# Kernel tuning notes

Measured on AMD Instinct MI355X. Metric: run time of the kernel, lower is better.

## Reference

```python
import jax, jax.numpy as jnp
import numpy as np
from jax import lax

# --- config (matches init_kwargs) ---
H = 1024          # hidden_size
I = 704           # moe_intermediate_size (per expert)
E = 32            # n_routed_experts
G = 8             # n_group
TOPK_GROUP = 3    # topk_group
K = 6             # num_experts_per_tok
N_SHARED = 2      # n_shared_experts -> shared intermediate = N_SHARED * I
SCALE = 1.0       # routed_scaling_factor
T = 2048          # number of tokens
CAP = 2 * (T * K) // E


def setup_inputs() -> dict:
    key = jax.random.key(0)
    ks = jax.random.split(key, 8)
    s = 0.02  # initializer_range
    Is = N_SHARED * I
    return {
        "x": jax.random.normal(ks[0], (T, H), jnp.float32),
        "gate_w": s * jax.random.normal(ks[1], (E, H), jnp.float32),   # router
        "w_gate": s * jax.random.normal(ks[2], (E, H, I), jnp.float32),
        "w_up":   s * jax.random.normal(ks[3], (E, H, I), jnp.float32),
        "w_down": s * jax.random.normal(ks[4], (E, I, H), jnp.float32),
        "sw_gate": s * jax.random.normal(ks[5], (H, Is), jnp.float32),
        "sw_up":   s * jax.random.normal(ks[6], (H, Is), jnp.float32),
        "sw_down": s * jax.random.normal(ks[7], (Is, H), jnp.float32),
    }


def _moe_forward(x, gate_w, w_gate, w_up, w_down, sw_gate, sw_up, sw_down):
    # ---- router: softmax scores + group-limited top-k (topk_method='gready') ----
    logits = x @ gate_w.T                                  # [T, E]
    scores = jax.nn.softmax(logits, axis=-1)               # [T, E]
    group_scores = scores.reshape(T, G, E // G).max(-1)    # [T, G]
    _, gidx = lax.top_k(group_scores, TOPK_GROUP)          # [T, topk_group]
    gmask = jnp.zeros((T, G), scores.dtype).at[jnp.arange(T)[:, None], gidx].set(1.0)
    emask = jnp.repeat(gmask, E // G, axis=1)              # [T, E]
    masked_scores = jnp.where(emask > 0, scores, 0.0)
    topk_w, topk_idx = lax.top_k(masked_scores, K)         # [T, K]
    # norm_topk_prob=False -> weights are raw softmax scores * routed_scaling_factor
    topk_w = topk_w * SCALE

    # ---- dispatch: sort assignments by expert, scatter into [E, CAP, H] buffers ----
    flat_e = topk_idx.reshape(-1)                          # [T*K]
    order = jnp.argsort(flat_e)
    se = flat_e[order]                                     # sorted expert ids
    tok = order // K                                       # source token of each slot
    counts = jax.ops.segment_sum(jnp.ones_like(flat_e), flat_e, num_segments=E)
    starts = jnp.cumsum(counts) - counts
    pos = jnp.arange(T * K) - starts[se]                   # position within expert
    valid = pos < CAP
    pos_w = jnp.where(valid, pos, CAP)                     # overflow slot CAP (sliced off)
    xbuf = jnp.zeros((E, CAP + 1, H), x.dtype).at[se, pos_w].set(x[tok])
    xb = xbuf[:, :CAP]                                     # [E, CAP, H]

    # ---- grouped expert MLPs: silu(x Wg) * (x Wu) @ Wd ----
    g = jnp.einsum("ech,ehi->eci", xb, w_gate)
    u = jnp.einsum("ech,ehi->eci", xb, w_up)
    yb = jnp.einsum("eci,eih->ech", jax.nn.silu(g) * u, w_down)  # [E, CAP, H]

    # ---- combine: gather back and weighted-scatter to tokens ----
    y_flat = yb[se, jnp.minimum(pos, CAP - 1)] * valid[:, None].astype(x.dtype)
    wts = topk_w.reshape(-1)[order]                        # [T*K]
    routed = jnp.zeros((T, H), x.dtype).at[tok].add(y_flat * wts[:, None])

    # ---- shared experts MLP (intermediate = n_shared * moe_inter) ----
    sg = jax.nn.silu(x @ sw_gate) * (x @ sw_up)
    shared = sg @ sw_down

    return routed + shared                                 # [T, H]


def reference(x, gate_w, w_gate, w_up, w_down, sw_gate, sw_up, sw_down):
    return _moe_forward(x, gate_w, w_gate, w_up, w_down, sw_gate, sw_up, sw_down)
```

## Files before the change

### kernel.cpp

```cpp
#include <hip/hip_runtime.h>
#include <hip/hip_bf16.h>

#define H 1024
#define I_DIM 704
#define E 32
#define TOPK_GROUP 3
#define K_TOP 6
#define T_TOK 2048
#define CAP 768
#define IS_DIM 1408
#define NCHUNK 192

typedef __attribute__((ext_vector_type(8))) short short8v;
typedef __attribute__((ext_vector_type(4))) float f32x4;

__device__ __forceinline__ unsigned short f2bfbits(float f) {
  unsigned u = __float_as_uint(f);
  unsigned r = (u + 0x7fffu + ((u >> 16) & 1u)) >> 16;
  return (unsigned short)r;
}
__device__ __forceinline__ unsigned packbf2(float lo, float hi) {
  __hip_bfloat162 h = __float22bfloat162_rn(make_float2(lo, hi));
  unsigned u; __builtin_memcpy(&u, &h, 4); return u;
}
__device__ __forceinline__ float bf2f(unsigned short b) {
  return __uint_as_float(((unsigned)b) << 16);
}
__device__ __forceinline__ void gload_lds16(const short* g, short* l) {
  __builtin_amdgcn_global_load_lds(
      (const __attribute__((address_space(1))) unsigned int*)g,
      (__attribute__((address_space(3))) unsigned int*)l, 16, 0, 0);
}

__global__ void cast_x_kernel(const float* __restrict__ x, short* __restrict__ xb) {
  size_t i = ((size_t)blockIdx.x * 256 + threadIdx.x) * 4;
  float4 v = *(const float4*)(x + i);
  short4 s;
  s.x = (short)f2bfbits(v.x); s.y = (short)f2bfbits(v.y);
  s.z = (short)f2bfbits(v.z); s.w = (short)f2bfbits(v.w);
  *(short4*)(xb + i) = s;
}

__global__ __launch_bounds__(64) void gating_kernel(const float* __restrict__ x,
                                                    const float* __restrict__ gw,
                                                    int* __restrict__ tidx,
                                                    float* __restrict__ tw) {
  int t = blockIdx.x;
  int lane = threadIdx.x;
  int e = lane & 31, half = lane >> 5;
  const float4* xr4 = (const float4*)(x + (size_t)t * H + half * 512);
  const float4* wr4 = (const float4*)(gw + (size_t)e * H + half * 512);
  double acc = 0.0;
  #pragma unroll 4
  for (int j = 0; j < 128; ++j) {
    float4 a = xr4[j], b = wr4[j];
    acc += (double)a.x * b.x + (double)a.y * b.y + (double)a.z * b.z + (double)a.w * b.w;
  }
  acc += __shfl_down(acc, 32);
  double lg = acc;
  double m = lg;
  #pragma unroll
  for (int off = 16; off >= 1; off >>= 1) {
    double o = __shfl_xor(m, off);
    if (o > m) m = o;
  }
  double p = exp(lg - m);
  double sum = p;
  #pragma unroll
  for (int off = 16; off >= 1; off >>= 1) sum += __shfl_xor(sum, off);
  p /= sum;
  double gmax = p;
  { double o = __shfl_xor(gmax, 1); if (o > gmax) gmax = o;
    o = __shfl_xor(gmax, 2); if (o > gmax) gmax = o; }
  bool gsel = false;
  double gv = gmax;
  #pragma unroll
  for (int it = 0; it < TOPK_GROUP; ++it) {
    double v = gv; int gi = e >> 2;
    #pragma unroll
    for (int off = 16; off >= 1; off >>= 1) {
      double ov = __shfl_xor(v, off);
      int oi = __shfl_xor(gi, off);
      if (ov > v || (ov == v && oi < gi)) { v = ov; gi = oi; }
    }
    if ((e >> 2) == gi) { gsel = true; gv = -1e300; }
  }
  double mp = gsel ? p : 0.0;
  #pragma unroll
  for (int it = 0; it < K_TOP; ++it) {
    double v = mp; int ei = e;
    #pragma unroll
    for (int off = 16; off >= 1; off >>= 1) {
      double ov = __shfl_xor(v, off);
      int oi = __shfl_xor(ei, off);
      if (ov > v || (ov == v && oi < ei)) { v = ov; ei = oi; }
    }
    if (lane == 0) { tidx[t * K_TOP + it] = ei; tw[t * K_TOP + it] = (float)v; }
    if (e == ei) mp = -2.0;
  }
}

__global__ __launch_bounds__(64) void hist_kernel(const int* __restrict__ tidx,
                                                  int* __restrict__ chunk_hist) {
  __shared__ int h[E];
  int c = blockIdx.x, lane = threadIdx.x;
  if (lane < E) h[lane] = 0;
  __syncthreads();
  int te = tidx[c * 64 + lane];
  atomicAdd(&h[te], 1);
  __syncthreads();
  if (lane < E) chunk_hist[c * E + lane] = h[lane];
}

__global__ __launch_bounds__(1024) void scan_kernel(const int* __restrict__ chunk_hist,
                                                    int* __restrict__ chunk_base,
                                                    int* __restrict__ cnt) {
  __shared__ int h[NCHUNK * E];
  int t = threadIdx.x;
  for (int i = t; i < NCHUNK * E; i += 1024) h[i] = chunk_hist[i];
  __syncthreads();
  if (t < E) {
    int run = 0;
    for (int c = 0; c < NCHUNK; ++c) {
      int v = h[c * E + t];
      h[c * E + t] = run;
      run += v;
    }
    cnt[t] = run < CAP ? run : CAP;
  }
  __syncthreads();
  for (int i = t; i < NCHUNK * E; i += 1024) chunk_base[i] = h[i];
}

__global__ __launch_bounds__(64) void place_kernel(const int* __restrict__ tidx,
                                                   const int* __restrict__ chunk_base,
                                                   int* __restrict__ token_list,
                                                   int* __restrict__ sid) {
  int c = blockIdx.x, lane = threadIdx.x;
  int idx = c * 64 + lane;
  int te = tidx[idx];
  unsigned long long mymask = 0;
  #pragma unroll
  for (int e = 0; e < E; ++e) {
    unsigned long long bal = __ballot(te == e);
    if (te == e) mymask = bal;
  }
  int rank = __popcll(mymask & ((1ull << lane) - 1ull));
  int pos = chunk_base[c * E + te] + rank;
  int s = -1;
  if (pos < CAP) {
    token_list[te * CAP + pos] = idx / K_TOP;
    s = te * CAP + pos;
  }
  sid[idx] = s;
}

__global__ __launch_bounds__(256) void gateup_kernel(
    const short* __restrict__ Xb, const float* __restrict__ Wg, const float* __restrict__ Wu,
    short* __restrict__ Sout, const int* __restrict__ tlist, const int* __restrict__ cnt_dev,
    int Nld, long long wstride, long long sstride) {
  int e = blockIdx.z;
  int cnt = cnt_dev ? cnt_dev[e] : T_TOK;
  int row0 = blockIdx.y * 128;
  if (row0 >= cnt) return;
  int col0 = blockIdx.x * 64;
  const float* wg = Wg + (long long)e * wstride;
  const float* wu = Wu + (long long)e * wstride;
  short* sbase = Sout + (long long)e * sstride;

  __shared__ __align__(16) short As[2][128 * 32];
  __shared__ __align__(16) short Bgs[64 * 32];
  __shared__ __align__(16) short Bus[64 * 32];

  int tid = threadIdx.x;
  int lane = tid & 63, wave = tid >> 6;

  int rr = tid >> 2, ch = tid & 3;
  int che = ch ^ ((rr >> 1) & 3);
  int ra0 = row0 + rr, ra1 = ra0 + 64;
  if (tlist) {
    const int* tl = tlist + e * CAP;
    ra0 = tl[min(ra0, cnt - 1)];
    ra1 = tl[min(ra1, cnt - 1)];
  }
  const short* pa0 = Xb + (size_t)ra0 * H + che * 8;
  const short* pa1 = Xb + (size_t)ra1 * H + che * 8;
  short* ldsA00 = &As[0][(wave * 16) * 32];
  short* ldsA10 = &As[0][(64 + wave * 16) * 32];
  short* ldsA01 = &As[1][(wave * 16) * 32];
  short* ldsA11 = &As[1][(64 + wave * 16) * 32];

  int bn = lane;
  const float* pg = wg + (size_t)(wave * 8) * Nld + col0 + bn;
  const float* pu = wu + (size_t)(wave * 8) * Nld + col0 + bn;
  int kswz = (wave ^ ((bn >> 1) & 3)) * 8;
  short* ldsBg = &Bgs[bn * 32 + kswz];
  short* ldsBu = &Bus[bn * 32 + kswz];

  int wm = wave & 1, wn = wave >> 1;
  int c = lane & 15, q = lane >> 4;
  int qa = q ^ ((c >> 1) & 3);
  const short* fA0 = &As[0][(wm * 64 + c) * 32 + qa * 8];
  const short* fA1 = &As[1][(wm * 64 + c) * 32 + qa * 8];
  const short* fBg = &Bgs[(wn * 32 + c) * 32 + qa * 8];
  const short* fBu = &Bus[(wn * 32 + c) * 32 + qa * 8];

  f32x4 accg[4][2], accu[4][2];
  #pragma unroll
  for (int i = 0; i < 4; ++i)
    #pragma unroll
    for (int j = 0; j < 2; ++j) {
      accg[i][j] = (f32x4){0.f, 0.f, 0.f, 0.f};
      accu[i][j] = (f32x4){0.f, 0.f, 0.f, 0.f};
    }

  float gvA[8], uvA[8], gvB[8], uvB[8];
  gload_lds16(pa0, ldsA00);
  gload_lds16(pa1, ldsA10);
  #pragma unroll
  for (int j = 0; j < 8; ++j) {
    gvA[j] = pg[(size_t)j * Nld];
    uvA[j] = pu[(size_t)j * Nld];
  }

#define GU_PHASE(KC, FAC, LA0, LA1, GC, UC, GN, UN, PREF)                           \
  {                                                                                 \
    __builtin_amdgcn_s_barrier();                                                   \
    asm volatile("" ::: "memory");                                                  \
    if (PREF) {                                                                     \
      gload_lds16(pa0 + (KC) + 32, LA0);                                            \
      gload_lds16(pa1 + (KC) + 32, LA1);                                            \
      const float* pgk = pg + (size_t)((KC) + 32) * Nld;                            \
      const float* puk = pu + (size_t)((KC) + 32) * Nld;                            \
      _Pragma("unroll")                                                             \
      for (int j = 0; j < 8; ++j) {                                                 \
        GN[j] = pgk[(size_t)j * Nld];                                               \
        UN[j] = puk[(size_t)j * Nld];                                               \
      }                                                                             \
    }                                                                               \
    uint4 wvg, wvu;                                                                 \
    wvg.x = packbf2(GC[0], GC[1]); wvg.y = packbf2(GC[2], GC[3]);                   \
    wvg.z = packbf2(GC[4], GC[5]); wvg.w = packbf2(GC[6], GC[7]);                   \
    wvu.x = packbf2(UC[0], UC[1]); wvu.y = packbf2(UC[2], UC[3]);                   \
    wvu.z = packbf2(UC[4], UC[5]); wvu.w = packbf2(UC[6], UC[7]);                   \
    *(uint4*)ldsBg = wvg;                                                           \
    *(uint4*)ldsBu = wvu;                                                           \
    asm volatile("s_waitcnt lgkmcnt(0)" ::: "memory");                              \
    asm volatile("s_waitcnt vmcnt(18)" ::: "memory");                               \
    __builtin_amdgcn_s_barrier();                                                   \
    __builtin_amdgcn_sched_barrier(0);                                              \
    short8v a[4], bg[2], bu[2];                                                     \
    _Pragma("unroll")                                                               \
    for (int mi = 0; mi < 4; ++mi) a[mi] = *(const short8v*)((FAC) + mi * 16 * 32); \
    _Pragma("unroll")                                                               \
    for (int ni = 0; ni < 2; ++ni) {                                                \
      bg[ni] = *(const short8v*)(fBg + ni * 16 * 32);                               \
      bu[ni] = *(const short8v*)(fBu + ni * 16 * 32);                               \
    }                                                                               \
    _Pragma("unroll")                                                               \
    for (int mi = 0; mi < 4; ++mi)                                                  \
      _Pragma("unroll")                                                             \
      for (int ni = 0; ni < 2; ++ni) {                                              \
        accg[mi][ni] = __builtin_amdgcn_mfma_f32_16x16x32_bf16(a[mi], bg[ni], accg[mi][ni], 0, 0, 0); \
        accu[mi][ni] = __builtin_amdgcn_mfma_f32_16x16x32_bf16(a[mi], bu[ni], accu[mi][ni], 0, 0, 0); \
      }                                                                             \
  }

  for (int k0 = 0; k0 < H; k0 += 64) {
    GU_PHASE(k0,      fA0, ldsA01, ldsA11, gvA, uvA, gvB, uvB, true);
    GU_PHASE(k0 + 32, fA1, ldsA00, ldsA10, gvB, uvB, gvA, uvA, (k0 + 64 < H));
  }
#undef GU_PHASE

  #pragma unroll
  for (int mi = 0; mi < 4; ++mi) {
    int rbase = row0 + wm * 64 + mi * 16 + q * 4;
    #pragma unroll
    for (int ni = 0; ni < 2; ++ni) {
      int col = col0 + wn * 32 + ni * 16 + c;
      #pragma unroll
      for (int r = 0; r < 4; ++r) {
        float g = accg[mi][ni][r], u = accu[mi][ni][r];
        float s = (g / (1.f + __expf(-g))) * u;
        sbase[(size_t)(rbase + r) * Nld + col] = (short)f2bfbits(s);
      }
    }
  }
}

__global__ __launch_bounds__(256) void down_kernel(
    const short* __restrict__ Sin, const float* __restrict__ Wd,
    float* __restrict__ outF, short* __restrict__ outY,
    const int* __restrict__ cnt_dev, int Kdim, long long wstride, long long sstride) {
  int e = blockIdx.z;
  int cnt = cnt_dev ? cnt_dev[e] : T_TOK;
  int row0 = blockIdx.y * 128;
  if (row0 >= cnt) return;
  int col0 = blockIdx.x * 128;
  const short* sb = Sin + (long long)e * sstride;
  const float* wd = Wd + (long long)e * wstride;

  __shared__ __align__(16) short As[2][128 * 32];
  __shared__ __align__(16) short Bs[128 * 32];

  int tid = threadIdx.x;
  int lane = tid & 63, wave = tid >> 6;
  int rr = tid >> 2, ch = tid & 3;
  int che = ch ^ ((rr >> 1) & 3);

  const short* pa0 = sb + (size_t)(row0 + rr) * Kdim + che * 8;
  const short* pa1 = pa0 + (size_t)64 * Kdim;
  short* ldsA00 = &As[0][(wave * 16) * 32];
  short* ldsA10 = &As[0][(64 + wave * 16) * 32];
  short* ldsA01 = &As[1][(wave * 16) * 32];
  short* ldsA11 = &As[1][(64 + wave * 16) * 32];

  int bn = tid & 127, w2 = tid >> 7;
  const float* pb = wd + (size_t)(w2 * 16) * H + col0 + bn;
  int bs = (bn >> 1) & 3;
  short* ldsB0 = &Bs[bn * 32 + ((w2 * 2) ^ bs) * 8];
  short* ldsB1 = &Bs[bn * 32 + ((w2 * 2 + 1) ^ bs) * 8];

  int wm = wave & 1, wn = wave >> 1;
  int c = lane & 15, q = lane >> 4;
  int qa = q ^ ((c >> 1) & 3);
  const short* fA0 = &As[0][(wm * 64 + c) * 32 + qa * 8];
  const short* fA1 = &As[1][(wm * 64 + c) * 32 + qa * 8];
  const short* fB  = &Bs[(wn * 64 + c) * 32 + qa * 8];

  f32x4 acc[4][4];
  #pragma unroll
  for (int i = 0; i < 4; ++i)
    #pragma unroll
    for (int j = 0; j < 4; ++j) acc[i][j] = (f32x4){0.f, 0.f, 0.f, 0.f};

  float bvA[16], bvB[16];
  gload_lds16(pa0, ldsA00);
  gload_lds16(pa1, ldsA10);
  #pragma unroll
  for (int j = 0; j < 16; ++j) bvA[j] = pb[(size_t)j * H];

#define DN_PHASE(KC, FAC, LA0, LA1, BC, BND, PREF)                                  \
  {                                                                                 \
    __builtin_amdgcn_s_barrier();                                                   \
    asm volatile("" ::: "memory");                                                  \
    if (PREF) {                                                                     \
      gload_lds16(pa0 + (KC) + 32, LA0);                                            \
      gload_lds16(pa1 + (KC) + 32, LA1);                                            \
      const float* pbk = pb + (size_t)((KC) + 32) * H;                              \
      _Pragma("unroll")                                                             \
      for (int j = 0; j < 16; ++j) BND[j] = pbk[(size_t)j * H];                     \
    }                                                                               \
    uint4 w0, w1;                                                                   \
    w0.x = packbf2(BC[0], BC[1]);   w0.y = packbf2(BC[2], BC[3]);                   \
    w0.z = packbf2(BC[4], BC[5]);   w0.w = packbf2(BC[6], BC[7]);                   \
    w1.x = packbf2(BC[8], BC[9]);   w1.y = packbf2(BC[10], BC[11]);                 \
    w1.z = packbf2(BC[12], BC[13]); w1.w = packbf2(BC[14], BC[15]);                 \
    *(uint4*)ldsB0 = w0;                                                            \
    *(uint4*)ldsB1 = w1;                                                            \
    asm volatile("s_waitcnt lgkmcnt(0)" ::: "memory");                              \
    asm volatile("s_waitcnt vmcnt(18)" ::: "memory");                               \
    __builtin_amdgcn_s_barrier();                                                   \
    __builtin_amdgcn_sched_barrier(0);                                              \
    short8v a[4], b[4];                                                             \
    _Pragma("unroll")                                                               \
    for (int mi = 0; mi < 4; ++mi) a[mi] = *(const short8v*)((FAC) + mi * 16 * 32); \
    _Pragma("unroll")                                                               \
    for (int ni = 0; ni < 4; ++ni) b[ni] = *(const short8v*)(fB + ni * 16 * 32);    \
    _Pragma("unroll")                                                               \
    for (int mi = 0; mi < 4; ++mi)                                                  \
      _Pragma("unroll")                                                             \
      for (int ni = 0; ni < 4; ++ni)                                                \
        acc[mi][ni] = __builtin_amdgcn_mfma_f32_16x16x32_bf16(a[mi], b[ni], acc[mi][ni], 0, 0, 0); \
  }

  for (int k0 = 0; k0 < Kdim; k0 += 64) {
    DN_PHASE(k0,      fA0, ldsA01, ldsA11, bvA, bvB, true);
    DN_PHASE(k0 + 32, fA1, ldsA00, ldsA10, bvB, bvA, (k0 + 64 < Kdim));
  }
#undef DN_PHASE

  if (outY) {
    #pragma unroll
    for (int mi = 0; mi < 4; ++mi) {
      int rb = row0 + wm * 64 + mi * 16 + q * 4;
      #pragma unroll
      for (int r = 0; r < 4; ++r) {
        short* yrow = outY + (size_t)(e * CAP + rb + r) * H;
        #pragma unroll
        for (int ni = 0; ni < 4; ++ni) {
          int col = col0 + wn * 64 + ni * 16 + c;
          yrow[col] = (short)f2bfbits(acc[mi][ni][r]);
        }
      }
    }
  } else {
    #pragma unroll
    for (int mi = 0; mi < 4; ++mi) {
      int rb = row0 + wm * 64 + mi * 16 + q * 4;
      #pragma unroll
      for (int ni = 0; ni < 4; ++ni) {
        int col = col0 + wn * 64 + ni * 16 + c;
        #pragma unroll
        for (int r = 0; r < 4; ++r)
          outF[(size_t)(rb + r) * H + col] = acc[mi][ni][r];
      }
    }
  }
}

__global__ __launch_bounds__(256) void combine_kernel(
    const short* __restrict__ Yr, const int* __restrict__ sid,
    const float* __restrict__ twt, float* __restrict__ out) {
  int t = blockIdx.x;
  int col = threadIdx.x * 4;
  float* op = out + (size_t)t * H + col;
  float4 o = *(float4*)op;
  #pragma unroll
  for (int k = 0; k < K_TOP; ++k) {
    int s = sid[t * K_TOP + k];
    if (s >= 0) {
      float w = twt[t * K_TOP + k];
      ushort4 y = *(const ushort4*)(Yr + (size_t)s * H + col);
      o.x += w * bf2f(y.x);
      o.y += w * bf2f(y.y);
      o.z += w * bf2f(y.z);
      o.w += w * bf2f(y.w);
    }
  }
  *(float4*)op = o;
}

extern "C" void kernel_launch(void* const* d_in, const int* in_sizes, int n_in,
                              void* d_out, int out_size, void* d_ws, size_t ws_size,
                              hipStream_t stream) {
  const float* x       = (const float*)d_in[0];
  const float* gate_w  = (const float*)d_in[1];
  const float* w_gate  = (const float*)d_in[2];
  const float* w_up    = (const float*)d_in[3];
  const float* w_down  = (const float*)d_in[4];
  const float* sw_gate = (const float*)d_in[5];
  const float* sw_up   = (const float*)d_in[6];
  const float* sw_down = (const float*)d_in[7];
  float* out = (float*)d_out;
  char* ws = (char*)d_ws;

  size_t o = 0;
  short* xb   = (short*)(ws + o); o += (size_t)T_TOK * H * 2;
  short* Sr   = (short*)(ws + o); o += (size_t)E * CAP * I_DIM * 2;
  short* Ss   = (short*)(ws + o); o += (size_t)T_TOK * IS_DIM * 2;
  short* Yr   = (short*)(ws + o); o += (size_t)E * CAP * H * 2;
  int*   tidx = (int*)(ws + o);   o += (size_t)T_TOK * K_TOP * 4;
  float* twt  = (float*)(ws + o); o += (size_t)T_TOK * K_TOP * 4;
  int*   sid  = (int*)(ws + o);   o += (size_t)T_TOK * K_TOP * 4;
  int*   tl   = (int*)(ws + o);   o += (size_t)E * CAP * 4;
  int*   cnt  = (int*)(ws + o);   o += 256;
  int*   chist = (int*)(ws + o);  o += (size_t)NCHUNK * E * 4;
  int*   cbase = (int*)(ws + o);  o += (size_t)NCHUNK * E * 4;

  cast_x_kernel<<<(T_TOK * H) / 1024, 256, 0, stream>>>(x, xb);
  gating_kernel<<<T_TOK, 64, 0, stream>>>(x, gate_w, tidx, twt);
  hist_kernel<<<NCHUNK, 64, 0, stream>>>(tidx, chist);
  scan_kernel<<<1, 1024, 0, stream>>>(chist, cbase, cnt);
  place_kernel<<<NCHUNK, 64, 0, stream>>>(tidx, cbase, tl, sid);

  gateup_kernel<<<dim3(I_DIM / 64, CAP / 128, E), 256, 0, stream>>>(
      xb, w_gate, w_up, Sr, tl, cnt, I_DIM, (long long)H * I_DIM, (long long)CAP * I_DIM);
  gateup_kernel<<<dim3(IS_DIM / 64, T_TOK / 128, 1), 256, 0, stream>>>(
      xb, sw_gate, sw_up, Ss, nullptr, nullptr, IS_DIM, 0, 0);
  down_kernel<<<dim3(H / 128, T_TOK / 128, 1), 256, 0, stream>>>(
      Ss, sw_down, out, nullptr, nullptr, IS_DIM, 0, 0);
  down_kernel<<<dim3(H / 128, CAP / 128, E), 256, 0, stream>>>(
      Sr, w_down, nullptr, Yr, cnt, I_DIM, (long long)I_DIM * H, (long long)CAP * I_DIM);
  combine_kernel<<<T_TOK, 256, 0, stream>>>(Yr, sid, twt, out);
}
```

Measured before the change: 548.0 us.

## Pre-transpose weights to bf16 and stream B tiles via direct-to-LDS loads

Adds a tiled transpose-and-cast kernel that converts every expert and shared weight matrix from fp32 [K,N] to bf16 [N,K] on each call. The gate/up and down GEMMs then load B tiles with the same global_load_lds path as A, double-buffered in LDS. This removes the per-thread strided fp32 loads, register staging and bf16 packing from the GEMM inner loop. The cost is an extra full pass over all weights every call, plus more workspace, with the transposed gate weights aliased onto the Yr buffer.

```diff
diff --git a/kernel.cpp b/kernel.cpp
--- a/kernel.cpp
+++ b/kernel.cpp
@@ -19,10 +19,6 @@
   unsigned r = (u + 0x7fffu + ((u >> 16) & 1u)) >> 16;
   return (unsigned short)r;
 }
-__device__ __forceinline__ unsigned packbf2(float lo, float hi) {
-  __hip_bfloat162 h = __float22bfloat162_rn(make_float2(lo, hi));
-  unsigned u; __builtin_memcpy(&u, &h, 4); return u;
-}
 __device__ __forceinline__ float bf2f(unsigned short b) {
   return __uint_as_float(((unsigned)b) << 16);
 }
@@ -39,6 +35,38 @@
   s.x = (short)f2bfbits(v.x); s.y = (short)f2bfbits(v.y);
   s.z = (short)f2bfbits(v.z); s.w = (short)f2bfbits(v.w);
   *(short4*)(xb + i) = s;
+}
+
+__global__ __launch_bounds__(256) void tw_kernel(const float* __restrict__ in,
+                                                 short* __restrict__ out,
+                                                 int K, int N) {
+  __shared__ float tile[64][65];
+  long long eoff = (long long)blockIdx.z * (long long)K * N;
+  const float* ip = in + eoff;
+  short* op = out + eoff;
+  int n0 = blockIdx.x * 64, k0 = blockIdx.y * 64;
+  int t = threadIdx.x;
+  int tr = t >> 4;
+  int tc = (t & 15) * 4;
+  #pragma unroll
+  for (int i = 0; i < 4; ++i) {
+    float4 v = *(const float4*)(ip + (size_t)(k0 + tr + i * 16) * N + n0 + tc);
+    tile[tr + i * 16][tc + 0] = v.x;
+    tile[tr + i * 16][tc + 1] = v.y;
+    tile[tr + i * 16][tc + 2] = v.z;
+    tile[tr + i * 16][tc + 3] = v.w;
+  }
+  __syncthreads();
+  #pragma unroll
+  for (int i = 0; i < 4; ++i) {
+    int n = tr + i * 16;
+    short4 s;
+    s.x = (short)f2bfbits(tile[tc + 0][n]);
+    s.y = (short)f2bfbits(tile[tc + 1][n]);
+    s.z = (short)f2bfbits(tile[tc + 2][n]);
+    s.w = (short)f2bfbits(tile[tc + 3][n]);
+    *(short4*)(op + (size_t)(n0 + n) * K + k0 + tc) = s;
+  }
 }
 
 __global__ __launch_bounds__(64) void gating_kernel(const float* __restrict__ x,
@@ -156,7 +184,7 @@
 }
 
 __global__ __launch_bounds__(256) void gateup_kernel(
-    const short* __restrict__ Xb, const float* __restrict__ Wg, const float* __restrict__ Wu,
+    const short* __restrict__ Xb, const short* __restrict__ Wg, const short* __restrict__ Wu,
     short* __restrict__ Sout, const int* __restrict__ tlist, const int* __restrict__ cnt_dev,
     int Nld, long long wstride, long long sstride) {
   int e = blockIdx.z;
@@ -164,13 +192,13 @@
   int row0 = blockIdx.y * 128;
   if (row0 >= cnt) return;
   int col0 = blockIdx.x * 64;
-  const float* wg = Wg + (long long)e * wstride;
-  const float* wu = Wu + (long long)e * wstride;
+  const short* wg = Wg + (long long)e * wstride;
+  const short* wu = Wu + (long long)e * wstride;
   short* sbase = Sout + (long long)e * sstride;
 
   __shared__ __align__(16) short As[2][128 * 32];
-  __shared__ __align__(16) short Bgs[64 * 32];
-  __shared__ __align__(16) short Bus[64 * 32];
+  __shared__ __align__(16) short Bgs[2][64 * 32];
+  __shared__ __align__(16) short Bus[2][64 * 32];
 
   int tid = threadIdx.x;
   int lane = tid & 63, wave = tid >> 6;
@@ -185,25 +213,27 @@
   }
   const short* pa0 = Xb + (size_t)ra0 * H + che * 8;
   const short* pa1 = Xb + (size_t)ra1 * H + che * 8;
+  const short* pbg = wg + (size_t)(col0 + rr) * H + che * 8;
+  const short* pbu = wu + (size_t)(col0 + rr) * H + che * 8;
+
   short* ldsA00 = &As[0][(wave * 16) * 32];
   short* ldsA10 = &As[0][(64 + wave * 16) * 32];
   short* ldsA01 = &As[1][(wave * 16) * 32];
   short* ldsA11 = &As[1][(64 + wave * 16) * 32];
-
-  int bn = lane;
-  const float* pg = wg + (size_t)(wave * 8) * Nld + col0 + bn;
-  const float* pu = wu + (size_t)(wave * 8) * Nld + col0 + bn;
-  int kswz = (wave ^ ((bn >> 1) & 3)) * 8;
-  short* ldsBg = &Bgs[bn * 32 + kswz];
-  short* ldsBu = &Bus[bn * 32 + kswz];
+  short* ldsBg0 = &Bgs[0][(wave * 16) * 32];
+  short* ldsBg1 = &Bgs[1][(wave * 16) * 32];
+  short* ldsBu0 = &Bus[0][(wave * 16) * 32];
+  short* ldsBu1 = &Bus[1][(wave * 16) * 32];
 
   int wm = wave & 1, wn = wave >> 1;
   int c = lane & 15, q = lane >> 4;
   int qa = q ^ ((c >> 1) & 3);
-  const short* fA0 = &As[0][(wm * 64 + c) * 32 + qa * 8];
-  const short* fA1 = &As[1][(wm * 64 + c) * 32 + qa * 8];
-  const short* fBg = &Bgs[(wn * 32 + c) * 32 + qa * 8];
-  const short* fBu = &Bus[(wn * 32 + c) * 32 + qa * 8];
+  const short* fA0  = &As[0][(wm * 64 + c) * 32 + qa * 8];
+  const short* fA1  = &As[1][(wm * 64 + c) * 32 + qa * 8];
+  const short* fBg0 = &Bgs[0][(wn * 32 + c) * 32 + qa * 8];
+  const short* fBg1 = &Bgs[1][(wn * 32 + c) * 32 + qa * 8];
+  const short* fBu0 = &Bus[0][(wn * 32 + c) * 32 + qa * 8];
+  const short* fBu1 = &Bus[1][(wn * 32 + c) * 32 + qa * 8];
 
   f32x4 accg[4][2], accu[4][2];
   #pragma unroll
@@ -214,48 +244,33 @@
       accu[i][j] = (f32x4){0.f, 0.f, 0.f, 0.f};
     }
 
-  float gvA[8], uvA[8], gvB[8], uvB[8];
   gload_lds16(pa0, ldsA00);
   gload_lds16(pa1, ldsA10);
-  #pragma unroll
-  for (int j = 0; j < 8; ++j) {
-    gvA[j] = pg[(size_t)j * Nld];
-    uvA[j] = pu[(size_t)j * Nld];
-  }
-
-#define GU_PHASE(KC, FAC, LA0, LA1, GC, UC, GN, UN, PREF)                           \
+  gload_lds16(pbg, ldsBg0);
+  gload_lds16(pbu, ldsBu0);
+
+#define GU_PHASE(KC, FAc, FBGc, FBUc, A0d, A1d, BGd, BUd, PREF)                     \
   {                                                                                 \
     __builtin_amdgcn_s_barrier();                                                   \
     asm volatile("" ::: "memory");                                                  \
     if (PREF) {                                                                     \
-      gload_lds16(pa0 + (KC) + 32, LA0);                                            \
-      gload_lds16(pa1 + (KC) + 32, LA1);                                            \
-      const float* pgk = pg + (size_t)((KC) + 32) * Nld;                            \
-      const float* puk = pu + (size_t)((KC) + 32) * Nld;                            \
-      _Pragma("unroll")                                                             \
-      for (int j = 0; j < 8; ++j) {                                                 \
-        GN[j] = pgk[(size_t)j * Nld];                                               \
-        UN[j] = puk[(size_t)j * Nld];                                               \
-      }                                                                             \
+      gload_lds16(pa0 + (KC) + 32, A0d);                                            \
+      gload_lds16(pa1 + (KC) + 32, A1d);                                            \
+      gload_lds16(pbg + (KC) + 32, BGd);                                            \
+      gload_lds16(pbu + (KC) + 32, BUd);                                            \
+      asm volatile("s_waitcnt vmcnt(4)" ::: "memory");                              \
+    } else {                                                                        \
+      asm volatile("s_waitcnt vmcnt(0)" ::: "memory");                              \
     }                                                                               \
-    uint4 wvg, wvu;                                                                 \
-    wvg.x = packbf2(GC[0], GC[1]); wvg.y = packbf2(GC[2], GC[3]);                   \
-    wvg.z = packbf2(GC[4], GC[5]); wvg.w = packbf2(GC[6], GC[7]);                   \
-    wvu.x = packbf2(UC[0], UC[1]); wvu.y = packbf2(UC[2], UC[3]);                   \
-    wvu.z = packbf2(UC[4], UC[5]); wvu.w = packbf2(UC[6], UC[7]);                   \
-    *(uint4*)ldsBg = wvg;                                                           \
-    *(uint4*)ldsBu = wvu;                                                           \
-    asm volatile("s_waitcnt lgkmcnt(0)" ::: "memory");                              \
-    asm volatile("s_waitcnt vmcnt(18)" ::: "memory");                               \
     __builtin_amdgcn_s_barrier();                                                   \
     __builtin_amdgcn_sched_barrier(0);                                              \
     short8v a[4], bg[2], bu[2];                                                     \
     _Pragma("unroll")                                                               \
-    for (int mi = 0; mi < 4; ++mi) a[mi] = *(const short8v*)((FAC) + mi * 16 * 32); \
+    for (int mi = 0; mi < 4; ++mi) a[mi] = *(const short8v*)((FAc) + mi * 16 * 32); \
     _Pragma("unroll")                                                               \
     for (int ni = 0; ni < 2; ++ni) {                                                \
-      bg[ni] = *(const short8v*)(fBg + ni * 16 * 32);                               \
-      bu[ni] = *(const short8v*)(fBu + ni * 16 * 32);                               \
+      bg[ni] = *(const short8v*)((FBGc) + ni * 16 * 32);                            \
+      bu[ni] = *(const short8v*)((FBUc) + ni * 16 * 32);                            \
     }                                                                               \
     _Pragma("unroll")                                                               \
     for (int mi = 0; mi < 4; ++mi)                                                  \
@@ -267,8 +282,8 @@
   }
 
   for (int k0 = 0; k0 < H; k0 += 64) {
-    GU_PHASE(k0,      fA0, ldsA01, ldsA11, gvA, uvA, gvB, uvB, true);
-    GU_PHASE(k0 + 32, fA1, ldsA00, ldsA10, gvB, uvB, gvA, uvA, (k0 + 64 < H));
+    GU_PHASE(k0,      fA0, fBg0, fBu0, ldsA01, ldsA11, ldsBg1, ldsBu1, true);
+    GU_PHASE(k0 + 32, fA1, fBg1, fBu1, ldsA00, ldsA10, ldsBg0, ldsBu0, (k0 + 64 < H));
   }
 #undef GU_PHASE
 
@@ -289,7 +304,7 @@
 }
 
 __global__ __launch_bounds__(256) void down_kernel(
-    const short* __restrict__ Sin, const float* __restrict__ Wd,
+    const short* __restrict__ Sin, const short* __restrict__ Wd,
     float* __restrict__ outF, short* __restrict__ outY,
     const int* __restrict__ cnt_dev, int Kdim, long long wstride, long long sstride) {
   int e = blockIdx.z;
@@ -298,10 +313,10 @@
   if (row0 >= cnt) return;
   int col0 = blockIdx.x * 128;
   const short* sb = Sin + (long long)e * sstride;
-  const float* wd = Wd + (long long)e * wstride;
+  const short* wd = Wd + (long long)e * wstride;
 
   __shared__ __align__(16) short As[2][128 * 32];
-  __shared__ __align__(16) short Bs[128 * 32];
+  __shared__ __align__(16) short Bs[2][128 * 32];
 
   int tid = threadIdx.x;
   int lane = tid & 63, wave = tid >> 6;
@@ -310,23 +325,25 @@
 
   const short* pa0 = sb + (size_t)(row0 + rr) * Kdim + che * 8;
   const short* pa1 = pa0 + (size_t)64 * Kdim;
+  const short* pb0 = wd + (size_t)(col0 + rr) * Kdim + che * 8;
+  const short* pb1 = pb0 + (size_t)64 * Kdim;
+
   short* ldsA00 = &As[0][(wave * 16) * 32];
   short* ldsA10 = &As[0][(64 + wave * 16) * 32];
   short* ldsA01 = &As[1][(wave * 16) * 32];
   short* ldsA11 = &As[1][(64 + wave * 16) * 32];
-
-  int bn = tid & 127, w2 = tid >> 7;
-  const float* pb = wd + (size_t)(w2 * 16) * H + col0 + bn;
-  int bs = (bn >> 1) & 3;
-  short* ldsB0 = &Bs[bn * 32 + ((w2 * 2) ^ bs) * 8];
-  short* ldsB1 = &Bs[bn * 32 + ((w2 * 2 + 1) ^ bs) * 8];
+  short* ldsB00 = &Bs[0][(wave * 16) * 32];
+  short* ldsB10 = &Bs[0][(64 + wave * 16) * 32];
+  short* ldsB01 = &Bs[1][(wave * 16) * 32];
+  short* ldsB11 = &Bs[1][(64 + wave * 16) * 32];
 
   int wm = wave & 1, wn = wave >> 1;
   int c = lane & 15, q = lane >> 4;
   int qa = q ^ ((c >> 1) & 3);
   const short* fA0 = &As[0][(wm * 64 + c) * 32 + qa * 8];
   const short* fA1 = &As[1][(wm * 64 + c) * 32 + qa * 8];
-  const short* fB  = &Bs[(wn * 64 + c) * 32 + qa * 8];
+  const short* fB0 = &Bs[0][(wn * 64 + c) * 32 + qa * 8];
+  const short* fB1 = &Bs[1][(wn * 64 + c) * 32 + qa * 8];
 
   f32x4 acc[4][4];
   #pragma unroll
@@ -334,39 +351,31 @@
     #pragma unroll
     for (int j = 0; j < 4; ++j) acc[i][j] = (f32x4){0.f, 0.f, 0.f, 0.f};
 
-  float bvA[16], bvB[16];
   gload_lds16(pa0, ldsA00);
   gload_lds16(pa1, ldsA10);
-  #pragma unroll
-  for (int j = 0; j < 16; ++j) bvA[j] = pb[(size_t)j * H];
-
-#define DN_PHASE(KC, FAC, LA0, LA1, BC, BND, PREF)                                  \
+  gload_lds16(pb0, ldsB00);
+  gload_lds16(pb1, ldsB10);
+
+#define DN_PHASE(KC, FAc, FBc, A0d, A1d, B0d, B1d, PREF)                            \
   {                                                                                 \
     __builtin_amdgcn_s_barrier();                                                   \
     asm volatile("" ::: "memory");                                                  \
     if (PREF) {                                                                     \
-      gload_lds16(pa0 + (KC) + 32, LA0);                                            \
-      gload_lds16(pa1 + (KC) + 32, LA1);                                            \
-      const float* pbk = pb + (size_t)((KC) + 32) * H;                              \
-      _Pragma("unroll")                                                             \
-      for (int j = 0; j < 16; ++j) BND[j] = pbk[(size_t)j * H];                     \
+      gload_lds16(pa0 + (KC) + 32, A0d);                                            \
+      gload_lds16(pa1 + (KC) + 32, A1d);                                            \
+      gload_lds16(pb0 + (KC) + 32, B0d);                                            \
+      gload_lds16(pb1 + (KC) + 32, B1d);                                            \
+      asm volatile("s_waitcnt vmcnt(4)" ::: "memory");                              \
+    } else {                                                                        \
+      asm volatile("s_waitcnt vmcnt(0)" ::: "memory");                              \
     }                                                                               \
-    uint4 w0, w1;                                                                   \
-    w0.x = packbf2(BC[0], BC[1]);   w0.y = packbf2(BC[2], BC[3]);                   \
-    w0.z = packbf2(BC[4], BC[5]);   w0.w = packbf2(BC[6], BC[7]);                   \
-    w1.x = packbf2(BC[8], BC[9]);   w1.y = packbf2(BC[10], BC[11]);                 \
-    w1.z = packbf2(BC[12], BC[13]); w1.w = packbf2(BC[14], BC[15]);                 \
-    *(uint4*)ldsB0 = w0;                                                            \
-    *(uint4*)ldsB1 = w1;                                                            \
-    asm volatile("s_waitcnt lgkmcnt(0)" ::: "memory");                              \
-    asm volatile("s_waitcnt vmcnt(18)" ::: "memory");                               \
     __builtin_amdgcn_s_barrier();                                                   \
     __builtin_amdgcn_sched_barrier(0);                                              \
     short8v a[4], b[4];                                                             \
     _Pragma("unroll")                                                               \
-    for (int mi = 0; mi < 4; ++mi) a[mi] = *(const short8v*)((FAC) + mi * 16 * 32); \
-    _Pragma("unroll")                                                               \
-    for (int ni = 0; ni < 4; ++ni) b[ni] = *(const short8v*)(fB + ni * 16 * 32);    \
+    for (int mi = 0; mi < 4; ++mi) a[mi] = *(const short8v*)((FAc) + mi * 16 * 32); \
+    _Pragma("unroll")                                                               \
+    for (int ni = 0; ni < 4; ++ni) b[ni] = *(const short8v*)((FBc) + ni * 16 * 32); \
     _Pragma("unroll")                                                               \
     for (int mi = 0; mi < 4; ++mi)                                                  \
       _Pragma("unroll")                                                             \
@@ -375,8 +384,8 @@
   }
 
   for (int k0 = 0; k0 < Kdim; k0 += 64) {
-    DN_PHASE(k0,      fA0, ldsA01, ldsA11, bvA, bvB, true);
-    DN_PHASE(k0 + 32, fA1, ldsA00, ldsA10, bvB, bvA, (k0 + 64 < Kdim));
+    DN_PHASE(k0,      fA0, fB0, ldsA01, ldsA11, ldsB01, ldsB11, true);
+    DN_PHASE(k0 + 32, fA1, fB1, ldsA00, ldsA10, ldsB00, ldsB10, (k0 + 64 < Kdim));
   }
 #undef DN_PHASE
 
@@ -449,7 +458,13 @@
   short* xb   = (short*)(ws + o); o += (size_t)T_TOK * H * 2;
   short* Sr   = (short*)(ws + o); o += (size_t)E * CAP * I_DIM * 2;
   short* Ss   = (short*)(ws + o); o += (size_t)T_TOK * IS_DIM * 2;
-  short* Yr   = (short*)(ws + o); o += (size_t)E * CAP * H * 2;
+  short* wg_t = (short*)(ws + o);
+  short* Yr   = (short*)(ws + o); o += (size_t)E * H * I_DIM * 2;
+  short* wu_t = (short*)(ws + o); o += (size_t)E * H * I_DIM * 2;
+  short* wd_t = (short*)(ws + o); o += (size_t)E * I_DIM * H * 2;
+  short* swg_t = (short*)(ws + o); o += (size_t)H * IS_DIM * 2;
+  short* swu_t = (short*)(ws + o); o += (size_t)H * IS_DIM * 2;
+  short* swd_t = (short*)(ws + o); o += (size_t)IS_DIM * H * 2;
   int*   tidx = (int*)(ws + o);   o += (size_t)T_TOK * K_TOP * 4;
   float* twt  = (float*)(ws + o); o += (size_t)T_TOK * K_TOP * 4;
   int*   sid  = (int*)(ws + o);   o += (size_t)T_TOK * K_TOP * 4;
@@ -464,13 +479,20 @@
   scan_kernel<<<1, 1024, 0, stream>>>(chist, cbase, cnt);
   place_kernel<<<NCHUNK, 64, 0, stream>>>(tidx, cbase, tl, sid);
 
+  tw_kernel<<<dim3(I_DIM / 64, H / 64, E), 256, 0, stream>>>(w_gate, wg_t, H, I_DIM);
+  tw_kernel<<<dim3(I_DIM / 64, H / 64, E), 256, 0, stream>>>(w_up,   wu_t, H, I_DIM);
+  tw_kernel<<<dim3(H / 64, I_DIM / 64, E), 256, 0, stream>>>(w_down, wd_t, I_DIM, H);
+  tw_kernel<<<dim3(IS_DIM / 64, H / 64, 1), 256, 0, stream>>>(sw_gate, swg_t, H, IS_DIM);
+  tw_kernel<<<dim3(IS_DIM / 64, H / 64, 1), 256, 0, stream>>>(sw_up,   swu_t, H, IS_DIM);
+  tw_kernel<<<dim3(H / 64, IS_DIM / 64, 1), 256, 0, stream>>>(sw_down, swd_t, IS_DIM, H);
+
   gateup_kernel<<<dim3(I_DIM / 64, CAP / 128, E), 256, 0, stream>>>(
-      xb, w_gate, w_up, Sr, tl, cnt, I_DIM, (long long)H * I_DIM, (long long)CAP * I_DIM);
+      xb, wg_t, wu_t, Sr, tl, cnt, I_DIM, (long long)H * I_DIM, (long long)CAP * I_DIM);
   gateup_kernel<<<dim3(IS_DIM / 64, T_TOK / 128, 1), 256, 0, stream>>>(
-      xb, sw_gate, sw_up, Ss, nullptr, nullptr, IS_DIM, 0, 0);
+      xb, swg_t, swu_t, Ss, nullptr, nullptr, IS_DIM, 0, 0);
   down_kernel<<<dim3(H / 128, T_TOK / 128, 1), 256, 0, stream>>>(
-      Ss, sw_down, out, nullptr, nullptr, IS_DIM, 0, 0);
+      Ss, swd_t, out, nullptr, nullptr, IS_DIM, 0, 0);
   down_kernel<<<dim3(H / 128, CAP / 128, E), 256, 0, stream>>>(
-      Sr, w_down, nullptr, Yr, cnt, I_DIM, (long long)I_DIM * H, (long long)CAP * I_DIM);
+      Sr, wd_t, nullptr, Yr, cnt, I_DIM, (long long)I_DIM * H, (long long)CAP * I_DIM);
   combine_kernel<<<T_TOK, 256, 0, stream>>>(Yr, sid, twt, out);
 }
```

Measured after the change: 548.3 us. About the same (+0.1%).
